# Kernel tuning notes

Hardware: AMD Instinct MI355X
Metric: run time of the kernel (lower is better)

The kernel has to match this reference:

```python
import jax, jax.numpy as jnp
import numpy as np

D, DFF, H, V, BS, NL, NG = 1024, 4096, 16, 32000, 128, 2, 2

def _ln(x, w, b, eps=1e-5):
    m = x.mean(-1, keepdims=True)
    v = ((x - m) ** 2).mean(-1, keepdims=True)
    return (x - m) / jnp.sqrt(v + eps) * w + b

def _full_attn(q, k, v):
    # q,k,v: [B,H,S,dk] ; manual max-subtract softmax with +1e-9 denom and clamp, per FullAttention
    dk = q.shape[-1]
    s = jnp.einsum('bhqd,bhkd->bhqk', q / jnp.sqrt(jnp.float32(dk)), k)
    s = s - s.max(-1, keepdims=True)
    e = jnp.exp(s)
    a = e / (e.sum(-1, keepdims=True) + 1e-9)
    a = jnp.clip(a, 1e-9, 1.0)
    return jnp.einsum('bhqk,bhkd->bhqd', a, v)

def _attn_layer(qi, ki, vi, lnw, lnb, pw, pb):
    # lnw/lnb: [4,D] (norm_q,k,v,out); pw: [4,D,D] (q,k,v,o, stored [in,out]); pb: [4,D]
    B, Sq, _ = qi.shape
    Sk = ki.shape[1]
    q = _ln(qi, lnw[0], lnb[0]) @ pw[0] + pb[0]
    k = _ln(ki, lnw[1], lnb[1]) @ pw[1] + pb[1]
    v = _ln(vi, lnw[2], lnb[2]) @ pw[2] + pb[2]
    dk = D // H
    q = q.reshape(B, Sq, H, dk).transpose(0, 2, 1, 3)
    k = k.reshape(B, Sk, H, dk).transpose(0, 2, 1, 3)
    v = v.reshape(B, Sk, H, dk).transpose(0, 2, 1, 3)
    o = _full_attn(q, k, v).transpose(0, 2, 1, 3).reshape(B, Sq, D)
    o = o @ pw[3] + pb[3]
    return _ln(o, lnw[3], lnb[3])

def _ffn(x, n1w, n1b, n2w, n2b, w1, b1, w2, b2):
    h = jax.nn.gelu(_ln(x, n1w, n1b) @ w1 + b1, approximate=False)
    return _ln(h @ w2 + b2 + x, n2w, n2b)

def _tlayer(x, lnw, lnb, pw, pb, w1, b1, w2, b2):
    # lnw/lnb: [6,D] (attn q,k,v,out norms, ffn norm1, ffn norm2)
    x = x + _attn_layer(x, x, x, lnw[:4], lnb[:4], pw, pb)
    return _ffn(x, lnw[4], lnb[4], lnw[5], lnb[5], w1, b1, w2, b2)

def _pe(S, d):
    pos = jnp.arange(S, dtype=jnp.float32)[:, None]
    div = jnp.exp(jnp.arange(0, d, 2, dtype=jnp.float32) * (-np.log(10000.0) / d))
    pe = jnp.zeros((S, d), jnp.float32)
    pe = pe.at[:, 0::2].set(jnp.sin(pos * div))
    pe = pe.at[:, 1::2].set(jnp.cos(pos * div))
    return pe

def setup_inputs() -> dict:
    key = jax.random.key(0)
    ks = iter(jax.random.split(key, 64))
    nrm = lambda shp: jax.random.normal(next(ks), shp, jnp.float32) * 0.02
    inp = {
        'x': jax.random.randint(next(ks), (4, 4096), 0, V, dtype=jnp.int32).astype(jnp.int64),
        'emb': nrm((V, D)),
        'in_ln_w': jnp.ones((D,)), 'in_ln_b': jnp.zeros((D,)),
        'loc_ln_w': jnp.ones((NL, 6, D)), 'loc_ln_b': jnp.zeros((NL, 6, D)),
        'loc_pw': nrm((NL, 4, D, D)), 'loc_pb': jnp.zeros((NL, 4, D)),
        'loc_w1': nrm((NL, D, DFF)), 'loc_b1': jnp.zeros((NL, DFF)),
        'loc_w2': nrm((NL, DFF, D)), 'loc_b2': jnp.zeros((NL, D)),
        'locn_w': jnp.ones((D,)), 'locn_b': jnp.zeros((D,)),
        'pool_q': nrm((1, 1, D)),
        'pool_n_w': jnp.ones((D,)), 'pool_n_b': jnp.zeros((D,)),
        'pool_ln_w': jnp.ones((4, D)), 'pool_ln_b': jnp.zeros((4, D)),
        'pool_pw': nrm((4, D, D)), 'pool_pb': jnp.zeros((4, D)),
        'glob_ln_w': jnp.ones((NG, 6, D)), 'glob_ln_b': jnp.zeros((NG, 6, D)),
        'glob_pw': nrm((NG, 4, D, D)), 'glob_pb': jnp.zeros((NG, 4, D)),
        'glob_w1': nrm((NG, D, DFF)), 'glob_b1': jnp.zeros((NG, DFF)),
        'glob_w2': nrm((NG, DFF, D)), 'glob_b2': jnp.zeros((NG, D)),
        'out_ln_w': jnp.ones((D,)), 'out_ln_b': jnp.zeros((D,)),
        'out_w': nrm((D, V)), 'out_b': jnp.zeros((V,)),
    }
    return inp

def reference(x, emb, in_ln_w, in_ln_b, loc_ln_w, loc_ln_b, loc_pw, loc_pb,
              loc_w1, loc_b1, loc_w2, loc_b2, locn_w, locn_b,
              pool_q, pool_n_w, pool_n_b, pool_ln_w, pool_ln_b, pool_pw, pool_pb,
              glob_ln_w, glob_ln_b, glob_pw, glob_pb, glob_w1, glob_b1, glob_w2, glob_b2,
              out_ln_w, out_ln_b, out_w, out_b):
    B, S = x.shape
    nb = S // BS
    h = jnp.clip(emb[x], -100.0, 100.0) + _pe(S, D)[None]
    h = _ln(h, in_ln_w, in_ln_b)
    h = h.reshape(B * nb, BS, D)  # local blocks
    for i in range(NL):
        h = jnp.clip(_tlayer(h, loc_ln_w[i], loc_ln_b[i], loc_pw[i], loc_pb[i],
                             loc_w1[i], loc_b1[i], loc_w2[i], loc_b2[i]), -100.0, 100.0)
    h = _ln(h, locn_w, locn_b)
    # attention pooling of each block to one vector
    hp = _ln(h, pool_n_w, pool_n_b)
    q = jnp.broadcast_to(pool_q, (B * nb, 1, D))
    g = _attn_layer(q, hp, hp, pool_ln_w, pool_ln_b, pool_pw, pool_pb)[:, 0].reshape(B, nb, D)
    for i in range(NG):
        g = jnp.clip(_tlayer(g, glob_ln_w[i], glob_ln_b[i], glob_pw[i], glob_pb[i],
                             glob_w1[i], glob_b1[i], glob_w2[i], glob_b2[i]), -100.0, 100.0)
    g = _ln(g, out_ln_w, out_ln_b)
    return g @ out_w + out_b  # [B, num_blocks, vocab]
```

## Files before the change

kernel.cpp:

```cpp
#include <hip/hip_runtime.h>
#include <hip/hip_bf16.h>
#include <math.h>

#define DEV __device__ __forceinline__

typedef __attribute__((ext_vector_type(8))) short bf16x8;
typedef __attribute__((ext_vector_type(4))) float f32x4;
typedef unsigned short u16;

constexpr int D_ = 1024, NTOK = 16384, SEQ = 4096;

DEV u16 f2b(float f){
  union{float f;unsigned u;} v; v.f=f;
  unsigned r = (v.u + 0x7fffu + ((v.u>>16)&1u))>>16;
  return (u16)r;
}
DEV float b2f(u16 h){ union{unsigned u;float f;} v; v.u=((unsigned)h)<<16; return v.f; }

DEV float gelu_f(float x){
  float z = 0.7978845608028654f*(x + 0.044715f*x*x*x);
  float e = __expf(-2.f*z);
  float t = 2.f/(1.f+e) - 1.f;
  return 0.5f*x*(1.f+t);
}

DEV void gld16(const void* g, void* l){
  __builtin_amdgcn_global_load_lds((const __attribute__((address_space(1))) void*)g,
                                   (__attribute__((address_space(3))) void*)l, 16, 0, 0);
}

DEV float blockSum(float v){
  __shared__ float sb[4];
  #pragma unroll
  for(int m=32;m>=1;m>>=1) v += __shfl_xor(v, m, 64);
  int lane = threadIdx.x & 63, wv = threadIdx.x >> 6;
  __syncthreads();
  if(lane==0) sb[wv]=v;
  __syncthreads();
  float r = sb[0]+sb[1]+sb[2]+sb[3];
  __syncthreads();
  return r;
}

__global__ __launch_bounds__(256) void detect_k(const int* __restrict__ xr, int* __restrict__ flag){
  int tid=threadIdx.x; float cnt=0.f;
  for(int i=tid;i<8192;i+=256) if(xr[2*i+1]!=0) cnt+=1.f;
  cnt = blockSum(cnt);
  if(tid==0) *flag = (cnt < 64.f) ? 1 : 0;
}

__global__ __launch_bounds__(256) void embed_k(const void* __restrict__ xv, const int* __restrict__ flag,
      const float* __restrict__ emb, const float* __restrict__ w, const float* __restrict__ b,
      u16* __restrict__ out, u16* __restrict__ outn){
  int t = blockIdx.x;
  int id;
  if(*flag) id = (int)((const long long*)xv)[t];
  else      id = ((const int*)xv)[t];
  int s = t & (SEQ-1);
  int d0 = threadIdx.x*4;
  float4 e4 = *(const float4*)(emb + (size_t)id*D_ + d0);
  float vv[4] = {e4.x, e4.y, e4.z, e4.w};
  float acc = 0.f;
  #pragma unroll
  for(int i=0;i<4;i++){
    float e = fminf(fmaxf(vv[i], -100.f), 100.f);
    int d = d0+i;
    float fr = expf(-(float)(d & ~1) * (9.210340371976184f/(float)D_));
    float ang = (float)s * fr;
    e += (d&1) ? cosf(ang) : sinf(ang);
    vv[i]=e; acc+=e;
  }
  float mean = blockSum(acc)*(1.f/D_);
  float var=0.f;
  #pragma unroll
  for(int i=0;i<4;i++){ float dd=vv[i]-mean; var+=dd*dd; }
  var = blockSum(var)*(1.f/D_);
  float rs = rsqrtf(var+1e-5f);
  float y[4];
  #pragma unroll
  for(int i=0;i<4;i++) y[i] = (vv[i]-mean)*rs*w[d0+i]+b[d0+i];
  ushort4 o; o.x=f2b(y[0]); o.y=f2b(y[1]); o.z=f2b(y[2]); o.w=f2b(y[3]);
  *(ushort4*)(out + (size_t)t*D_ + d0) = o;
  float m2 = blockSum(y[0]+y[1]+y[2]+y[3])*(1.f/D_);
  float v2=0.f;
  #pragma unroll
  for(int i=0;i<4;i++){ float dd=y[i]-m2; v2+=dd*dd; }
  v2 = blockSum(v2)*(1.f/D_);
  float rs2 = rsqrtf(v2+1e-5f);
  ushort4 on; on.x=f2b((y[0]-m2)*rs2); on.y=f2b((y[1]-m2)*rs2); on.z=f2b((y[2]-m2)*rs2); on.w=f2b((y[3]-m2)*rs2);
  *(ushort4*)(outn + (size_t)t*D_ + d0) = on;
}

template<int MODE,int WRN>
__global__ __launch_bounds__(256) void ln_k(const u16* __restrict__ in, const u16* __restrict__ res,
      const float* __restrict__ w, const float* __restrict__ b, u16* __restrict__ out,
      u16* __restrict__ outn){
  int t = blockIdx.x; int d0 = threadIdx.x*4;
  ushort4 r4 = *(const ushort4*)(in + (size_t)t*D_ + d0);
  float vv[4] = {b2f(r4.x),b2f(r4.y),b2f(r4.z),b2f(r4.w)};
  float mean = blockSum(vv[0]+vv[1]+vv[2]+vv[3])*(1.f/D_);
  float var=0.f;
  #pragma unroll
  for(int i=0;i<4;i++){ float dd=vv[i]-mean; var+=dd*dd; }
  var = blockSum(var)*(1.f/D_);
  float rs = rsqrtf(var+1e-5f);
  float rv[4]={0,0,0,0};
  if(MODE==3){
    ushort4 q4 = *(const ushort4*)(res + (size_t)t*D_ + d0);
    rv[0]=b2f(q4.x); rv[1]=b2f(q4.y); rv[2]=b2f(q4.z); rv[3]=b2f(q4.w);
  }
  float y[4];
  #pragma unroll
  for(int i=0;i<4;i++){
    float v = (vv[i]-mean)*rs;
    v = v*w[d0+i]+b[d0+i];
    if(MODE==2) v = fminf(fmaxf(v,-100.f),100.f);
    if(MODE==3) v += rv[i];
    y[i]=v;
  }
  ushort4 o; o.x=f2b(y[0]); o.y=f2b(y[1]); o.z=f2b(y[2]); o.w=f2b(y[3]);
  *(ushort4*)(out + (size_t)t*D_ + d0) = o;
  if(WRN){
    float m2 = blockSum(y[0]+y[1]+y[2]+y[3])*(1.f/D_);
    float v2=0.f;
    #pragma unroll
    for(int i=0;i<4;i++){ float dd=y[i]-m2; v2+=dd*dd; }
    v2 = blockSum(v2)*(1.f/D_);
    float rs2 = rsqrtf(v2+1e-5f);
    ushort4 on; on.x=f2b((y[0]-m2)*rs2); on.y=f2b((y[1]-m2)*rs2); on.z=f2b((y[2]-m2)*rs2); on.w=f2b((y[3]-m2)*rs2);
    *(ushort4*)(outn + (size_t)t*D_ + d0) = on;
  }
}

__global__ __launch_bounds__(256) void ln3x_k(const u16* __restrict__ in,
    const float* __restrict__ w1,const float* __restrict__ b1,
    const float* __restrict__ w2,const float* __restrict__ b2, u16* __restrict__ out){
  int t=blockIdx.x, d0=threadIdx.x*4;
  ushort4 r4 = *(const ushort4*)(in + (size_t)t*D_ + d0);
  float vv[4]={b2f(r4.x),b2f(r4.y),b2f(r4.z),b2f(r4.w)};
  #pragma unroll
  for(int pass=0;pass<3;pass++){
    float mean = blockSum(vv[0]+vv[1]+vv[2]+vv[3])*(1.f/D_);
    float var=0.f;
    #pragma unroll
    for(int i=0;i<4;i++){ float dd=vv[i]-mean; var+=dd*dd; }
    var = blockSum(var)*(1.f/D_);
    float rs = rsqrtf(var+1e-5f);
    #pragma unroll
    for(int i=0;i<4;i++){
      float y=(vv[i]-mean)*rs;
      if(pass==0) y = y*w1[d0+i]+b1[d0+i];
      else if(pass==1) y = y*w2[d0+i]+b2[d0+i];
      vv[i]=y;
    }
  }
  ushort4 o;
  o.x=f2b(vv[0]); o.y=f2b(vv[1]); o.z=f2b(vv[2]); o.w=f2b(vv[3]);
  *(ushort4*)(out + (size_t)t*D_ + d0) = o;
}

__global__ __launch_bounds__(256) void lnrow_k(const float* __restrict__ x, const float* __restrict__ w,
      const float* __restrict__ b, float* __restrict__ out){
  int d0=threadIdx.x*4;
  float vv[4]={x[d0],x[d0+1],x[d0+2],x[d0+3]};
  float mean = blockSum(vv[0]+vv[1]+vv[2]+vv[3])*(1.f/D_);
  float var=0.f;
  #pragma unroll
  for(int i=0;i<4;i++){ float dd=vv[i]-mean; var+=dd*dd; }
  var = blockSum(var)*(1.f/D_);
  float rs = rsqrtf(var+1e-5f);
  #pragma unroll
  for(int i=0;i<4;i++) out[d0+i]=(vv[i]-mean)*rs*w[d0+i]+b[d0+i];
}

#define TF_BODY(W, ldW, lnw, Wt, Kd, n0, k0)                                 \
  {                                                                          \
    int ty = threadIdx.x>>6, tx = threadIdx.x&63;                            \
    _Pragma("unroll")                                                        \
    for(int p=0;p<16;p++){                                                   \
      int row = p*4+ty;                                                      \
      float sc = (lnw) ? (lnw)[(k0)+row] : 1.f;                              \
      T[row][tx] = (W)[(size_t)((k0)+row)*(ldW) + (n0)+tx]*sc;               \
    }                                                                        \
    __syncthreads();                                                         \
    _Pragma("unroll")                                                        \
    for(int p=0;p<16;p++){                                                   \
      int row = p*4+ty;                                                      \
      (Wt)[(size_t)((n0)+row)*(Kd) + (k0)+tx] = f2b(T[tx][row]);             \
    }                                                                        \
  }

__global__ __launch_bounds__(256) void tf_k(const float* __restrict__ W, int ldW,
      const float* __restrict__ lnw, u16* __restrict__ Wt, int Kd){
  __shared__ float T[64][65];
  int n0 = blockIdx.x*64, k0 = blockIdx.y*64;
  TF_BODY(W, ldW, lnw, Wt, Kd, n0, k0)
}

__global__ __launch_bounds__(256) void prep_tf_layer_k(const float* __restrict__ pw,
      const float* __restrict__ w1, const float* __restrict__ w2, const float* __restrict__ lw,
      u16* __restrict__ Wqk, u16* __restrict__ Wv, u16* __restrict__ Wo,
      u16* __restrict__ W1t, u16* __restrict__ W2t){
  __shared__ float T[64][65];
  int bid = blockIdx.x;
  const float* W; int ldW; const float* lnw; u16* Wt; int Kd, n0, k0;
  if(bid < 1024){
    int m = bid>>8, t = bid&255;
    n0 = (t&15)*64; k0 = (t>>4)*64;
    W = pw + (size_t)m*1024*1024; ldW = 1024; Kd = 1024;
    lnw = (m<3) ? lw + m*1024 : nullptr;
    Wt = (m==0)?Wqk : (m==1)?(Wqk+1024*1024) : (m==2)?Wv : Wo;
  } else if(bid < 2048){
    int t = bid-1024;
    n0 = (t&63)*64; k0 = (t>>6)*64;
    W = w1; ldW = 4096; Kd = 1024; lnw = lw+4*1024; Wt = W1t;
  } else {
    int t = bid-2048;
    n0 = (t&15)*64; k0 = (t>>4)*64;
    W = w2; ldW = 1024; Kd = 4096; lnw = nullptr; Wt = W2t;
  }
  TF_BODY(W, ldW, lnw, Wt, Kd, n0, k0)
}

__global__ __launch_bounds__(256) void prep_tf_pool_k(const float* __restrict__ pw,
      const float* __restrict__ lw, u16* __restrict__ PWkv, u16* __restrict__ PWo){
  __shared__ float T[64][65];
  int bid = blockIdx.x;
  int m = 1 + (bid>>8), t = bid&255;
  int n0 = (t&15)*64, k0 = (t>>4)*64;
  const float* W = pw + (size_t)m*1024*1024;
  const float* lnw = (m<3) ? lw + m*1024 : nullptr;
  u16* Wt = (m==1)?PWkv : (m==2)?(PWkv+1024*1024) : PWo;
  TF_BODY(W, 1024, lnw, Wt, 1024, n0, k0)
}

DEV void bias_body(const float* W, int ldW, int Kd, const float* lnb, float pbv, float* out){
  int tid = threadIdx.x;
  float chk = 0.f;
  if(lnb){ for(int k=tid;k<Kd;k+=256) chk += fabsf(lnb[k]); }
  chk = blockSum(chk);
  if(chk==0.f){ if(tid==0) *out = pbv; return; }
  float s=0.f;
  for(int k=tid;k<Kd;k+=256) s += lnb[k]*W[(size_t)k*ldW];
  s = blockSum(s);
  if(tid==0) *out = pbv + s;
}

__global__ __launch_bounds__(256) void bias_k(const float* __restrict__ W, int ldW,
      const float* __restrict__ lnb, const float* __restrict__ pb, float* __restrict__ out, int Kd){
  int j = blockIdx.x;
  bias_body(W + j, ldW, Kd, lnb, pb[j], out + j);
}

__global__ __launch_bounds__(256) void prep_bias_layer_k(const float* __restrict__ pw,
      const float* __restrict__ w1, const float* __restrict__ w2,
      const float* __restrict__ lb, const float* __restrict__ pb,
      const float* __restrict__ b1in, const float* __restrict__ b2in,
      float* __restrict__ Bqk, float* __restrict__ Bv, float* __restrict__ Bo,
      float* __restrict__ B1, float* __restrict__ B2){
  int j = blockIdx.x;
  const float* W; int ldW, Kd; const float* lnb; float pbv; float* out;
  const size_t MM = 1024ull*1024;
  if(j<2048){ int m=j>>10; int col=j&1023; W=pw+m*MM+col; ldW=1024; Kd=1024; lnb=lb+m*1024; pbv=pb[m*1024+col]; out=Bqk+j; }
  else if(j<3072){ int col=j-2048; W=pw+2*MM+col; ldW=1024; Kd=1024; lnb=lb+2*1024; pbv=pb[2*1024+col]; out=Bv+col; }
  else if(j<4096){ int col=j-3072; W=pw+3*MM+col; ldW=1024; Kd=1024; lnb=nullptr; pbv=pb[3*1024+col]; out=Bo+col; }
  else if(j<8192){ int col=j-4096; W=w1+col; ldW=4096; Kd=1024; lnb=lb+4*1024; pbv=b1in[col]; out=B1+col; }
  else { int col=j-8192; W=w2+col; ldW=1024; Kd=4096; lnb=nullptr; pbv=b2in[col]; out=B2+col; }
  bias_body(W, ldW, Kd, lnb, pbv, out);
}

__global__ __launch_bounds__(256) void prep_bias_pool_k(const float* __restrict__ pw,
      const float* __restrict__ lb, const float* __restrict__ pb,
      float* __restrict__ Pbkv, float* __restrict__ Pbo){
  int j = blockIdx.x;
  const size_t MM = 1024ull*1024;
  int m = 1 + (j>>10), col = j&1023;
  const float* lnb = (m<3) ? lb + m*1024 : nullptr;
  float* out = (m==1)?(Pbkv+col) : (m==2)?(Pbkv+1024+col) : (Pbo+col);
  bias_body(pw + m*MM + col, 1024, 1024, lnb, pb[m*1024+col], out);
}

__global__ __launch_bounds__(256) void matvec_k(const float* __restrict__ xn, const float* __restrict__ W,
      int ldW, const float* __restrict__ bias, float* __restrict__ out){
  int j=blockIdx.x, tid=threadIdx.x;
  float s=0.f;
  for(int k=tid;k<1024;k+=256) s += xn[k]*W[(size_t)k*ldW + j];
  s=blockSum(s);
  if(tid==0) out[j]=s+bias[j];
}

template<int EPI,int OUTF,int TV>
__global__ __launch_bounds__(256) void gemm_k(const u16* __restrict__ A, const u16* __restrict__ Bt,
      const float* __restrict__ bias, const u16* __restrict__ resid, void* __restrict__ Cout,
      int M, int N, int K, int ldc){
  __shared__ u16 SH[16384];
  int tid = threadIdx.x, lane = tid&63, wv = tid>>6;
  int g = lane>>4, l15 = lane&15;
  int GX = gridDim.x;
  int nwg = GX*gridDim.y;
  int flat = blockIdx.y*GX + blockIdx.x;
  int q = nwg>>3, r = nwg&7, xcd = flat&7, idx = flat>>3;
  int f = (xcd<r ? xcd*(q+1) : r*(q+1)+(xcd-r)*q) + idx;
  int by = f/GX, bx = f - by*GX;
  int row0 = by*128, col0 = bx*128;
  int wr = wv>>1, wc = wv&1;
  u16* As = SH;
  u16* Bs = SH + 8192;
  int e0 = wv*512 + lane*8;
  f32x4 acc[4][4] = {};
  auto STAGE = [&](int buf, int k0){
    #pragma unroll
    for(int c=0;c<2;c++){
      int e = c*2048 + e0;
      gld16(A  + (size_t)(row0 + (e>>5))*K + (k0 + (e&31)), &As[buf*4096 + e]);
      gld16(Bt + (size_t)(col0 + (e>>5))*K + (k0 + (e&31)), &Bs[buf*4096 + e]);
    }
  };
  STAGE(0, 0);
  int nt = K>>5;
  __syncthreads();
  int cur = 0;
  for(int t=0;t<nt;t++){
    if(t+1<nt) STAGE(cur^1, (t+1)<<5);
    bf16x8 a[4], b[4];
    #pragma unroll
    for(int m=0;m<4;m++) a[m] = *(const bf16x8*)&As[cur*4096 + (wr*64+m*16+l15)*32 + g*8];
    #pragma unroll
    for(int n=0;n<4;n++) b[n] = *(const bf16x8*)&Bs[cur*4096 + (wc*64+n*16+l15)*32 + g*8];
    #pragma unroll
    for(int m=0;m<4;m++)
      #pragma unroll
      for(int n=0;n<4;n++)
        acc[m][n] = __builtin_amdgcn_mfma_f32_16x16x32_bf16(a[m], b[n], acc[m][n], 0,0,0);
    __syncthreads();
    cur ^= 1;
  }
  if(TV){
    u16* Tb = SH;
    #pragma unroll
    for(int m=0;m<4;m++){
      #pragma unroll
      for(int n=0;n<4;n++){
        int c = wc*64 + n*16 + l15;
        float bs = bias[col0 + c];
        #pragma unroll
        for(int r2=0;r2<4;r2++){
          int Rl = wr*64 + m*16 + g*4 + r2;
          Tb[c*128 + (Rl ^ ((c&7)<<4))] = f2b(acc[m][n][r2]+bs);
        }
      }
    }
    __syncthreads();
    for(int p=tid*4; p<16384; p+=1024){
      int c = p>>7, rr = p&127;
      int rs = rr ^ ((c&7)<<4);
      ushort4 v4;
      v4.x = Tb[c*128+rs]; v4.y = Tb[c*128+rs+1]; v4.z = Tb[c*128+rs+2]; v4.w = Tb[c*128+rs+3];
      *(ushort4*)((u16*)Cout + (size_t)(col0+c)*M + row0 + rr) = v4;
    }
  } else {
    #pragma unroll
    for(int m=0;m<4;m++){
      #pragma unroll
      for(int n=0;n<4;n++){
        int Cc = col0 + wc*64 + n*16 + l15;
        float bs = bias[Cc];
        #pragma unroll
        for(int r2=0;r2<4;r2++){
          int R = row0 + wr*64 + m*16 + g*4 + r2;
          float v = acc[m][n][r2] + bs;
          if(EPI==1) v = gelu_f(v);
          if(EPI==2) v += b2f(resid[(size_t)R*ldc + Cc]);
          if(OUTF) ((float*)Cout)[(size_t)R*ldc + Cc] = v;
          else     ((u16*)Cout)[(size_t)R*ldc + Cc] = f2b(v);
        }
      }
    }
  }
}

__global__ __launch_bounds__(256) void attnl_k(const u16* __restrict__ QK, const u16* __restrict__ VT,
      u16* __restrict__ AT){
  __shared__ u16 SP[16384];
  __shared__ u16 Vt[8192];
  __shared__ float rmax[256], rsum[256];
  int tid=threadIdx.x, lane=tid&63, wv=tid>>6, g=lane>>4, l15=lane&15;
  int lb = blockIdx.x>>4, h = blockIdx.x&15;
  int wr=wv>>1, wc=wv&1;
  #pragma unroll
  for(int c=0;c<4;c++){
    int chunk = c*2048 + wv*512;
    int e = chunk + lane*8;
    gld16(QK + (size_t)(lb*128 + (e>>6))*2048 + h*64 + (e&63),        &SP[chunk]);
    gld16(QK + (size_t)(lb*128 + (e>>6))*2048 + 1024 + h*64 + (e&63), &SP[8192+chunk]);
    gld16(VT + (size_t)(h*64 + (e>>7))*16384 + lb*128 + (e&127),      &Vt[chunk]);
  }
  __syncthreads();
  f32x4 s[4][4] = {};
  #pragma unroll
  for(int ks=0;ks<2;ks++){
    bf16x8 a[4], b[4];
    #pragma unroll
    for(int m=0;m<4;m++) a[m] = *(const bf16x8*)&SP[(wr*64+m*16+l15)*64 + ks*32 + g*8];
    #pragma unroll
    for(int n=0;n<4;n++) b[n] = *(const bf16x8*)&SP[8192+(wc*64+n*16+l15)*64 + ks*32 + g*8];
    #pragma unroll
    for(int m=0;m<4;m++)
      #pragma unroll
      for(int n=0;n<4;n++)
        s[m][n] = __builtin_amdgcn_mfma_f32_16x16x32_bf16(a[m], b[n], s[m][n], 0,0,0);
  }
  #pragma unroll
  for(int m=0;m<4;m++)
    #pragma unroll
    for(int n=0;n<4;n++) s[m][n] *= 0.125f;
  #pragma unroll
  for(int m=0;m<4;m++)
    #pragma unroll
    for(int r=0;r<4;r++){
      float mx = fmaxf(fmaxf(s[m][0][r],s[m][1][r]),fmaxf(s[m][2][r],s[m][3][r]));
      #pragma unroll
      for(int msk=1;msk<16;msk<<=1) mx = fmaxf(mx, __shfl_xor(mx,msk,64));
      if(l15==0) rmax[(wr*64+m*16+g*4+r)*2+wc]=mx;
    }
  __syncthreads();
  #pragma unroll
  for(int m=0;m<4;m++)
    #pragma unroll
    for(int r=0;r<4;r++){
      int row = wr*64+m*16+g*4+r;
      float M2 = fmaxf(rmax[row*2], rmax[row*2+1]);
      float sm=0.f;
      #pragma unroll
      for(int n=0;n<4;n++){ float e = expf(s[m][n][r]-M2); s[m][n][r]=e; sm+=e; }
      #pragma unroll
      for(int msk=1;msk<16;msk<<=1) sm += __shfl_xor(sm,msk,64);
      if(l15==0) rsum[row*2+wc]=sm;
    }
  __syncthreads();
  #pragma unroll
  for(int m=0;m<4;m++)
    #pragma unroll
    for(int r=0;r<4;r++){
      int row = wr*64+m*16+g*4+r;
      float den = rsum[row*2]+rsum[row*2+1]+1e-9f;
      #pragma unroll
      for(int n=0;n<4;n++){
        float a = s[m][n][r]/den;
        a = fminf(fmaxf(a,1e-9f),1.f);
        SP[row*128 + wc*64+n*16+l15] = f2b(a);
      }
    }
  __syncthreads();
  f32x4 o[4][2] = {};
  #pragma unroll
  for(int ks=0;ks<4;ks++){
    bf16x8 a[4], b[2];
    #pragma unroll
    for(int m=0;m<4;m++) a[m] = *(const bf16x8*)&SP[(wr*64+m*16+l15)*128 + ks*32 + g*8];
    #pragma unroll
    for(int n=0;n<2;n++) b[n] = *(const bf16x8*)&Vt[(wc*32+n*16+l15)*128 + ks*32 + g*8];
    #pragma unroll
    for(int m=0;m<4;m++)
      #pragma unroll
      for(int n=0;n<2;n++)
        o[m][n] = __builtin_amdgcn_mfma_f32_16x16x32_bf16(a[m], b[n], o[m][n], 0,0,0);
  }
  #pragma unroll
  for(int m=0;m<4;m++)
    #pragma unroll
    for(int n=0;n<2;n++)
      #pragma unroll
      for(int r=0;r<4;r++)
        AT[(size_t)(lb*128 + wr*64+m*16+g*4+r)*1024 + h*64 + wc*32+n*16+l15] = f2b(o[m][n][r]);
}

__global__ __launch_bounds__(256) void poolattn_k(const float* __restrict__ qp, const u16* __restrict__ KV,
      u16* __restrict__ g0){
  int lb = blockIdx.x, tid = threadIdx.x;
  __shared__ float sc[16*128];
  for(int p=tid;p<2048;p+=256){
    int h=p>>7, j=p&127;
    const u16* krow = KV + (size_t)(lb*128+j)*2048 + h*64;
    float s=0.f;
    for(int d=0;d<64;d++) s += qp[h*64+d]*b2f(krow[d]);
    sc[h*128+j] = s*0.125f;
  }
  __syncthreads();
  if(tid<16){
    float* r=&sc[tid*128];
    float mx=r[0];
    for(int j=1;j<128;j++) mx=fmaxf(mx,r[j]);
    float sm=0.f;
    for(int j=0;j<128;j++){ float e=expf(r[j]-mx); r[j]=e; sm+=e; }
    sm+=1e-9f;
    for(int j=0;j<128;j++) r[j]=fminf(fmaxf(r[j]/sm,1e-9f),1.f);
  }
  __syncthreads();
  for(int c=tid;c<1024;c+=256){
    int h=c>>6;
    float acc=0.f;
    for(int j=0;j<128;j++) acc += sc[h*128+j]*b2f(KV[(size_t)(lb*128+j)*2048 + 1024 + c]);
    g0[(size_t)lb*1024 + c] = f2b(acc);
  }
}

__global__ __launch_bounds__(256) void attng_k(const u16* __restrict__ QKV, u16* __restrict__ OUT){
  int bb = blockIdx.x>>4, h = blockIdx.x&15;
  __shared__ float sc[32*32];
  int tid=threadIdx.x;
  for(int p=tid;p<1024;p+=256){
    int i=p>>5, j=p&31;
    const u16* q = QKV + (size_t)(bb*32+i)*3072 + h*64;
    const u16* k = QKV + (size_t)(bb*32+j)*3072 + 1024 + h*64;
    float s=0.f;
    for(int d=0;d<64;d++) s += b2f(q[d])*b2f(k[d]);
    sc[p] = s*0.125f;
  }
  __syncthreads();
  if(tid<32){
    float* r=&sc[tid*32];
    float mx=r[0];
    for(int j=1;j<32;j++) mx=fmaxf(mx,r[j]);
    float sm=0.f;
    for(int j=0;j<32;j++){ float e=expf(r[j]-mx); r[j]=e; sm+=e; }
    sm+=1e-9f;
    for(int j=0;j<32;j++) r[j]=fminf(fmaxf(r[j]/sm,1e-9f),1.f);
  }
  __syncthreads();
  for(int p=tid;p<2048;p+=256){
    int i=p>>6, d=p&63;
    float acc=0.f;
    for(int j=0;j<32;j++) acc += sc[i*32+j]*b2f(QKV[(size_t)(bb*32+j)*3072 + 2048 + h*64 + d]);
    OUT[(size_t)(bb*32+i)*1024 + h*64 + d] = f2b(acc);
  }
}

extern "C" void kernel_launch(void* const* d_in, const int* in_sizes, int n_in,
                              void* d_out, int out_size, void* d_ws, size_t ws_size,
                              hipStream_t stream) {
  (void)in_sizes; (void)n_in; (void)out_size;
  const void*  x       = d_in[0];
  const float* emb     = (const float*)d_in[1];
  const float* in_ln_w = (const float*)d_in[2];
  const float* in_ln_b = (const float*)d_in[3];
  const float* loc_ln_w= (const float*)d_in[4];
  const float* loc_ln_b= (const float*)d_in[5];
  const float* loc_pw  = (const float*)d_in[6];
  const float* loc_pb  = (const float*)d_in[7];
  const float* loc_w1  = (const float*)d_in[8];
  const float* loc_b1  = (const float*)d_in[9];
  const float* loc_w2  = (const float*)d_in[10];
  const float* loc_b2  = (const float*)d_in[11];
  const float* locn_w  = (const float*)d_in[12];
  const float* locn_b  = (const float*)d_in[13];
  const float* pool_q  = (const float*)d_in[14];
  const float* pool_n_w= (const float*)d_in[15];
  const float* pool_n_b= (const float*)d_in[16];
  const float* pool_ln_w=(const float*)d_in[17];
  const float* pool_ln_b=(const float*)d_in[18];
  const float* pool_pw = (const float*)d_in[19];
  const float* pool_pb = (const float*)d_in[20];
  const float* glob_ln_w=(const float*)d_in[21];
  const float* glob_ln_b=(const float*)d_in[22];
  const float* glob_pw = (const float*)d_in[23];
  const float* glob_pb = (const float*)d_in[24];
  const float* glob_w1 = (const float*)d_in[25];
  const float* glob_b1 = (const float*)d_in[26];
  const float* glob_w2 = (const float*)d_in[27];
  const float* glob_b2 = (const float*)d_in[28];
  const float* out_ln_w= (const float*)d_in[29];
  const float* out_ln_b= (const float*)d_in[30];
  const float* out_w   = (const float*)d_in[31];
  const float* out_b   = (const float*)d_in[32];

  char* wsb = (char*)d_ws;
  size_t off = 0;
  auto AL = [&](size_t n)->char*{ size_t o=(off+255)&~(size_t)255; off=o+n; return wsb+o; };

  int*  flag = (int*)AL(256);
  u16*  WA   = (u16*)AL(12ull*1024*1024*2);
  float* BA  = (float*)AL(12*1024*4);
  float* qn  = (float*)AL(1024*4);
  float* qp  = (float*)AL(1024*4);
  float* Hb  = (float*)AL(32000*4);
  u16*  R    = (u16*)AL(64ull*1024*1024*2);
  u16*  X    = (u16*)AL((size_t)NTOK*1024*2);
  u16*  XN   = (u16*)AL((size_t)NTOK*1024*2);
  u16*  G    = (u16*)AL(128ull*1024*2);
  u16*  GN   = (u16*)AL(128ull*1024*2);
  u16*  GQKV = (u16*)AL(128ull*3072*2);
  u16*  GAT  = (u16*)AL(128ull*1024*2);
  u16*  GO   = (u16*)AL(128ull*1024*2);
  u16*  GFH  = (u16*)AL(128ull*4096*2);
  u16*  g0   = (u16*)AL(128ull*1024*2);
  if(off > ws_size) return;

  u16 *LWqk = WA, *LWv = WA+2097152, *LWo = WA+3145728, *LW1 = WA+4194304, *LW2 = WA+8388608;
  float *Lbqk = BA, *Lbv = BA+2048, *Lbo = BA+3072, *Lb1 = BA+4096, *Lb2 = BA+8192;
  u16 *GWqkv = WA, *GWo = WA+3145728, *GW1 = WA+4194304, *GW2 = WA+8388608;
  float *Gbqkv = BA, *Gbo = BA+3072, *Gb1 = BA+4096, *Gb2 = BA+8192;
  u16 *PWkv = WA, *PWo = WA+2097152;
  float *Pbkv = BA, *Pbo = BA+2048;
  u16 *QKb = R, *VTb = R+33554432, *ATb = R+50331648;
  u16 *FH  = R;
  u16 *KVb = R;
  u16 *HW  = R;
  u16 *Ob  = XN;

  const size_t MM = 1024ull*1024;

  detect_k<<<1,256,0,stream>>>((const int*)x, flag);
  embed_k<<<NTOK,256,0,stream>>>(x, flag, emb, in_ln_w, in_ln_b, X, XN);

  for(int l=0;l<2;l++){
    const float* pw = loc_pw + (size_t)l*4*MM;
    const float* lw = loc_ln_w + (size_t)l*6*1024;
    const float* lb = loc_ln_b + (size_t)l*6*1024;
    const float* pb = loc_pb + (size_t)l*4*1024;
    const float* w1 = loc_w1 + (size_t)l*1024*4096;
    const float* w2 = loc_w2 + (size_t)l*4096*1024;
    prep_tf_layer_k<<<3072,256,0,stream>>>(pw, w1, w2, lw, LWqk, LWv, LWo, LW1, LW2);
    prep_bias_layer_k<<<9216,256,0,stream>>>(pw, w1, w2, lb, pb,
        loc_b1+(size_t)l*4096, loc_b2+(size_t)l*1024, Lbqk, Lbv, Lbo, Lb1, Lb2);

    gemm_k<0,0,0><<<dim3(16,128),256,0,stream>>>(XN, LWqk, Lbqk, nullptr, QKb, NTOK, 2048, 1024, 2048);
    gemm_k<0,0,1><<<dim3(8,128),256,0,stream>>>(XN, LWv, Lbv, nullptr, VTb, NTOK, 1024, 1024, 0);
    attnl_k<<<128*16,256,0,stream>>>(QKb, VTb, ATb);
    gemm_k<0,0,0><<<dim3(8,128),256,0,stream>>>(ATb, LWo, Lbo, nullptr, Ob, NTOK, 1024, 1024, 1024);
    ln_k<3,1><<<NTOK,256,0,stream>>>(Ob, X, lw+3*1024, lb+3*1024, X, XN);
    gemm_k<1,0,0><<<dim3(32,128),256,0,stream>>>(XN, LW1, Lb1, nullptr, FH, NTOK, 4096, 1024, 4096);
    gemm_k<2,0,0><<<dim3(8,128),256,0,stream>>>(FH, LW2, Lb2, X, Ob, NTOK, 1024, 4096, 1024);
    ln_k<2,1><<<NTOK,256,0,stream>>>(Ob, nullptr, lw+5*1024, lb+5*1024, X, XN);
  }

  prep_tf_pool_k<<<768,256,0,stream>>>(pool_pw, pool_ln_w, PWkv, PWo);
  prep_bias_pool_k<<<3072,256,0,stream>>>(pool_pw, pool_ln_b, pool_pb, Pbkv, Pbo);
  lnrow_k<<<1,256,0,stream>>>(pool_q, pool_ln_w, pool_ln_b, qn);
  matvec_k<<<1024,256,0,stream>>>(qn, pool_pw, 1024, pool_pb, qp);
  ln3x_k<<<NTOK,256,0,stream>>>(X, locn_w, locn_b, pool_n_w, pool_n_b, XN);
  gemm_k<0,0,0><<<dim3(16,128),256,0,stream>>>(XN, PWkv, Pbkv, nullptr, KVb, NTOK, 2048, 1024, 2048);
  poolattn_k<<<128,256,0,stream>>>(qp, KVb, g0);
  gemm_k<0,0,0><<<dim3(8,1),256,0,stream>>>(g0, PWo, Pbo, nullptr, GO, 128, 1024, 1024, 1024);
  ln_k<1,1><<<128,256,0,stream>>>(GO, nullptr, pool_ln_w+3*1024, pool_ln_b+3*1024, G, GN);

  for(int l=0;l<2;l++){
    const float* pw = glob_pw + (size_t)l*4*MM;
    const float* lw = glob_ln_w + (size_t)l*6*1024;
    const float* lb = glob_ln_b + (size_t)l*6*1024;
    const float* pb = glob_pb + (size_t)l*4*1024;
    const float* w1 = glob_w1 + (size_t)l*1024*4096;
    const float* w2 = glob_w2 + (size_t)l*4096*1024;
    prep_tf_layer_k<<<3072,256,0,stream>>>(pw, w1, w2, lw, GWqkv, GWqkv+2097152, GWo, GW1, GW2);
    prep_bias_layer_k<<<9216,256,0,stream>>>(pw, w1, w2, lb, pb,
        glob_b1+(size_t)l*4096, glob_b2+(size_t)l*1024, Gbqkv, Gbqkv+2048, Gbo, Gb1, Gb2);

    gemm_k<0,0,0><<<dim3(24,1),256,0,stream>>>(GN, GWqkv, Gbqkv, nullptr, GQKV, 128, 3072, 1024, 3072);
    attng_k<<<64,256,0,stream>>>(GQKV, GAT);
    gemm_k<0,0,0><<<dim3(8,1),256,0,stream>>>(GAT, GWo, Gbo, nullptr, GO, 128, 1024, 1024, 1024);
    ln_k<3,1><<<128,256,0,stream>>>(GO, G, lw+3*1024, lb+3*1024, G, GN);
    gemm_k<1,0,0><<<dim3(32,1),256,0,stream>>>(GN, GW1, Gb1, nullptr, GFH, 128, 4096, 1024, 4096);
    gemm_k<2,0,0><<<dim3(8,1),256,0,stream>>>(GFH, GW2, Gb2, G, GO, 128, 1024, 4096, 1024);
    ln_k<2,1><<<128,256,0,stream>>>(GO, nullptr, lw+5*1024, lb+5*1024, G, GN);
  }

  tf_k<<<dim3(500,16),256,0,stream>>>(out_w, 32000, out_ln_w, HW, 1024);
  bias_k<<<32000,256,0,stream>>>(out_w, 32000, out_ln_b, out_b, Hb, 1024);
  gemm_k<0,1,0><<<dim3(250,1),256,0,stream>>>(GN, HW, Hb, nullptr, d_out, 128, 32000, 1024, 32000);
}
```

Before: 2.158 ms.

## Triple-buffer GEMM LDS tiles with explicit vmcnt waits and single barrier

The bf16 GEMM main loop moves from double to triple buffering of A/B tiles in LDS, prefetching two K-steps ahead. It uses explicit s_waitcnt vmcnt(4)/lgkmcnt(0) plus a raw s_barrier instead of __syncthreads, so loads for the next-next tile can stay in flight across the barrier. This is meant to hide global-to-LDS latency better. In exchange it raises LDS use per block from 32KB to 48KB, which may reduce occupancy, and it depends on the hand-placed wait counts being correct.

```diff
diff --git a/kernel.cpp b/kernel.cpp
--- a/kernel.cpp
+++ b/kernel.cpp
@@ -28,6 +28,12 @@
   __builtin_amdgcn_global_load_lds((const __attribute__((address_space(1))) void*)g,
                                    (__attribute__((address_space(3))) void*)l, 16, 0, 0);
 }
+
+#define BAR()    __builtin_amdgcn_s_barrier()
+#define SCHED0() __builtin_amdgcn_sched_barrier(0)
+#define LGKM0()  asm volatile("s_waitcnt lgkmcnt(0)" ::: "memory")
+#define VM4()    asm volatile("s_waitcnt vmcnt(4)" ::: "memory")
+#define VM0()    asm volatile("s_waitcnt vmcnt(0)" ::: "memory")
 
 DEV float blockSum(float v){
   __shared__ float sb[4];
@@ -293,7 +299,7 @@
 __global__ __launch_bounds__(256) void gemm_k(const u16* __restrict__ A, const u16* __restrict__ Bt,
       const float* __restrict__ bias, const u16* __restrict__ resid, void* __restrict__ Cout,
       int M, int N, int K, int ldc){
-  __shared__ u16 SH[16384];
+  __shared__ u16 SH[24576];
   int tid = threadIdx.x, lane = tid&63, wv = tid>>6;
   int g = lane>>4, l15 = lane&15;
   int GX = gridDim.x;
@@ -304,38 +310,40 @@
   int by = f/GX, bx = f - by*GX;
   int row0 = by*128, col0 = bx*128;
   int wr = wv>>1, wc = wv&1;
-  u16* As = SH;
-  u16* Bs = SH + 8192;
   int e0 = wv*512 + lane*8;
   f32x4 acc[4][4] = {};
   auto STAGE = [&](int buf, int k0){
+    u16* base = SH + buf*8192;
     #pragma unroll
     for(int c=0;c<2;c++){
       int e = c*2048 + e0;
-      gld16(A  + (size_t)(row0 + (e>>5))*K + (k0 + (e&31)), &As[buf*4096 + e]);
-      gld16(Bt + (size_t)(col0 + (e>>5))*K + (k0 + (e&31)), &Bs[buf*4096 + e]);
+      gld16(A  + (size_t)(row0 + (e>>5))*K + (k0 + (e&31)), &base[e]);
+      gld16(Bt + (size_t)(col0 + (e>>5))*K + (k0 + (e&31)), &base[4096 + e]);
     }
   };
-  STAGE(0, 0);
   int nt = K>>5;
-  __syncthreads();
-  int cur = 0;
+  STAGE(0, 0); STAGE(1, 32);
+  VM4(); LGKM0(); BAR(); SCHED0();
   for(int t=0;t<nt;t++){
-    if(t+1<nt) STAGE(cur^1, (t+1)<<5);
-    bf16x8 a[4], b[4];
-    #pragma unroll
-    for(int m=0;m<4;m++) a[m] = *(const bf16x8*)&As[cur*4096 + (wr*64+m*16+l15)*32 + g*8];
-    #pragma unroll
-    for(int n=0;n<4;n++) b[n] = *(const bf16x8*)&Bs[cur*4096 + (wc*64+n*16+l15)*32 + g*8];
+    int b = t % 3;
+    if(t+2<nt) STAGE((t+2)%3, (t+2)<<5);
+    bf16x8 a[4], bb[4];
+    #pragma unroll
+    for(int m=0;m<4;m++) a[m] = *(const bf16x8*)&SH[b*8192 + (wr*64+m*16+l15)*32 + g*8];
+    #pragma unroll
+    for(int n=0;n<4;n++) bb[n] = *(const bf16x8*)&SH[b*8192 + 4096 + (wc*64+n*16+l15)*32 + g*8];
     #pragma unroll
     for(int m=0;m<4;m++)
       #pragma unroll
       for(int n=0;n<4;n++)
-        acc[m][n] = __builtin_amdgcn_mfma_f32_16x16x32_bf16(a[m], b[n], acc[m][n], 0,0,0);
+        acc[m][n] = __builtin_amdgcn_mfma_f32_16x16x32_bf16(a[m], bb[n], acc[m][n], 0,0,0);
+    if(t+1<nt){
+      if(t+2<nt){ VM4(); } else { VM0(); }
+      LGKM0(); BAR(); SCHED0();
+    }
+  }
+  if(TV){
     __syncthreads();
-    cur ^= 1;
-  }
-  if(TV){
     u16* Tb = SH;
     #pragma unroll
     for(int m=0;m<4;m++){
```

After: 2.097 ms. 2.8% less time.
